# Performance work log

Measured on AMD Instinct MI355X. Metric: run time of the kernel, lower is better.

The kernel has to match this reference:

```python
import jax, jax.numpy as jnp
import numpy as np

N_NODES = 100000
N_EDGES = 3200000
IN_CH = 128
HID_CH = 128
OUT_CH = 64
N_GRAPHS = 128


def gcn_conv(x, edge_index, edge_weight, W, b):
    # x: [N, F_in]; edge_index: [2, E] (row=source j, col=target i); edge_weight: [E]
    N = x.shape[0]
    x = x @ W  # [N, F_out]
    # add self-loops with weight 1 (PyG GCNConv default, fill_value=1.0)
    loop = jnp.arange(N, dtype=edge_index.dtype)
    row = jnp.concatenate([edge_index[0], loop])
    col = jnp.concatenate([edge_index[1], loop])
    w = jnp.concatenate([edge_weight, jnp.ones((N,), dtype=x.dtype)])
    # symmetric normalization: deg computed at target (col)
    deg = jax.ops.segment_sum(w, col, num_segments=N)
    dinv = jnp.where(deg > 0, jax.lax.rsqrt(deg), 0.0)
    norm = dinv[row] * w * dinv[col]  # [E+N]
    msg = x[row] * norm[:, None]  # gather + scale
    out = jax.ops.segment_sum(msg, col, num_segments=N)  # scatter-add
    return out + b


def setup_inputs() -> dict:
    key = jax.random.key(0)
    ks = jax.random.split(key, 10)
    x = jax.random.normal(ks[0], (N_NODES, IN_CH), dtype=jnp.float32)
    edge_index = jax.random.randint(ks[1], (2, N_EDGES), 0, N_NODES, dtype=jnp.int64)
    edge_attr = jax.random.uniform(ks[2], (N_EDGES,), dtype=jnp.float32)
    batch = jnp.sort(jax.random.randint(ks[3], (N_NODES,), 0, N_GRAPHS, dtype=jnp.int64))
    # GCNConv weights (glorot) and zero bias, classifier xavier_normal + bias 0.1
    def glorot(k, fi, fo):
        s = jnp.sqrt(6.0 / (fi + fo))
        return jax.random.uniform(k, (fi, fo), minval=-s, maxval=s, dtype=jnp.float32)
    W1 = glorot(ks[4], IN_CH, HID_CH)
    b1 = jnp.zeros((HID_CH,), dtype=jnp.float32)
    W2 = glorot(ks[5], HID_CH, HID_CH)
    b2 = jnp.zeros((HID_CH,), dtype=jnp.float32)
    std = jnp.sqrt(2.0 / (HID_CH + OUT_CH))
    Wc = jax.random.normal(ks[6], (HID_CH, OUT_CH), dtype=jnp.float32) * std
    bc = jnp.full((OUT_CH,), 0.1, dtype=jnp.float32)
    return {"x": x, "edge_index": edge_index, "edge_attr": edge_attr,
            "batch": batch, "W1": W1, "b1": b1, "W2": W2, "b2": b2,
            "Wc": Wc, "bc": bc}


def reference(x, edge_index, edge_attr, batch, W1, b1, W2, b2, Wc, bc):
    h = jax.nn.relu(gcn_conv(x, edge_index, edge_attr, W1, b1))
    h = jax.nn.relu(gcn_conv(h, edge_index, edge_attr, W2, b2))
    pooled = jax.ops.segment_sum(h, batch, num_segments=N_GRAPHS)  # [G, HID]
    logits = pooled @ Wc + bc
    return jax.nn.sigmoid(logits)
```

## Files before the change

### kernel.cpp

```cpp
#include <hip/hip_runtime.h>
#include <hip/hip_bf16.h>
#include <hip/hip_fp16.h>


#define FEAT 128
#define OUTC 64
#define NB_SHIFT 8
#define BINSZ 256
#define CAP 9216
#define TILE_A 8192
#define CNT_STRIDE 16
#define LDW 136

typedef _Float16 half8 __attribute__((ext_vector_type(8)));
typedef float    f32x4 __attribute__((ext_vector_type(4)));
typedef int      iv4  __attribute__((ext_vector_type(4)));

__global__ __launch_bounds__(256) void bin_edges(const int* __restrict__ ei,
                                                 const float* __restrict__ ew,
                                                 int* __restrict__ binCnt,
                                                 int2* __restrict__ binned,
                                                 int E, int nbins) {
    extern __shared__ int2 sE[];
    __shared__ int kh[512], kb[512], kc[512], kg[512], ksc[512];
    int tid = threadIdx.x;
    int e0 = blockIdx.x * TILE_A;
    kh[tid] = 0; kh[tid + 256] = 0;
    kc[tid] = 0; kc[tid + 256] = 0;
    __syncthreads();
    for (int i = 0; i < TILE_A; i += 256) {
        int e = e0 + i + tid;
        if (e < E) atomicAdd(&kh[ei[E + e] >> NB_SHIFT], 1);
    }
    __syncthreads();
    int v0 = kh[tid], v1 = kh[tid + 256];
    ksc[tid] = v0; ksc[tid + 256] = v1;
    __syncthreads();
    for (int off = 1; off < 512; off <<= 1) {
        int a0 = (tid >= off) ? ksc[tid - off] : 0;
        int a1 = (tid + 256 >= off) ? ksc[tid + 256 - off] : 0;
        __syncthreads();
        ksc[tid] += a0; ksc[tid + 256] += a1;
        __syncthreads();
    }
    kb[tid] = ksc[tid] - v0;
    kb[tid + 256] = ksc[tid + 256] - v1;
    if (tid < nbins && v0 > 0) kg[tid] = atomicAdd(&binCnt[tid * CNT_STRIDE], v0);
    int t2 = tid + 256;
    if (t2 < nbins && v1 > 0) kg[t2] = atomicAdd(&binCnt[t2 * CNT_STRIDE], v1);
    __syncthreads();
    for (int i = 0; i < TILE_A; i += 256) {
        int e = e0 + i + tid;
        if (e < E) {
            int col = ei[E + e];
            int row = ei[e];
            unsigned short hs = __half_as_ushort(__float2half(ew[e]));
            int b = col >> NB_SHIFT;
            int p = kb[b] + atomicAdd(&kc[b], 1);
            int cl = col & (BINSZ - 1);
            sE[p] = make_int2((cl << 24) | row, (b << 16) | (int)hs);
        }
    }
    __syncthreads();
    int tot = ksc[511];
    for (int i = tid; i < tot; i += 256) {
        int2 m = sE[i];
        int b = ((unsigned)m.y) >> 16;
        int loc = kg[b] + (i - kb[b]);
        if (loc < CAP)
            binned[(size_t)b * CAP + loc] = make_int2(m.x, m.y & 0xFFFF);
    }
}

__global__ __launch_bounds__(256) void bin_sort_csr(int2* __restrict__ binned,
                                                    const int* __restrict__ binCnt,
                                                    int* __restrict__ offs,
                                                    int* __restrict__ cnt,
                                                    float* __restrict__ dinv, int N) {
    extern __shared__ int2 sE[];
    __shared__ float dsum[BINSZ];
    __shared__ int kh[BINSZ], kb[BINSZ], ksc[BINSZ];
    int tid = threadIdx.x, b = blockIdx.x;
    int node0 = b << NB_SHIFT;
    dsum[tid] = 0.f;
    kh[tid] = 0;
    __syncthreads();
    int ne = min(binCnt[b * CNT_STRIDE], CAP);
    int2* src = binned + (size_t)b * CAP;
    for (int i = tid; i < ne; i += 256) {
        int2 m = src[i];
        int cl = ((unsigned)m.x) >> 24;
        atomicAdd(&kh[cl], 1);
        unsafeAtomicAdd(&dsum[cl], __half2float(__ushort_as_half((unsigned short)(m.y & 0xFFFF))));
    }
    __syncthreads();
    int v = kh[tid];
    ksc[tid] = v;
    __syncthreads();
    for (int off = 1; off < BINSZ; off <<= 1) {
        int t = (tid >= off) ? ksc[tid - off] : 0;
        __syncthreads();
        ksc[tid] += t;
        __syncthreads();
    }
    kb[tid] = ksc[tid] - v;
    kh[tid] = 0;
    __syncthreads();
    for (int i = tid; i < ne; i += 256) {
        int2 m = src[i];
        int cl = ((unsigned)m.x) >> 24;
        int p = kb[cl] + atomicAdd(&kh[cl], 1);
        int hw = m.y & 0xFFFF;
        sE[p] = make_int2(m.x & 0xFFFFFF, hw | (hw << 16));
    }
    __syncthreads();
    for (int i = tid; i < ne; i += 256) src[i] = sE[i];
    int node = node0 + tid;
    if (node < N) {
        offs[node] = b * CAP + kb[tid];
        cnt[node]  = kh[tid];
        dinv[node] = rsqrtf(1.0f + dsum[tid]);
    }
}

__global__ void wt_prep(const float* __restrict__ W, _Float16* __restrict__ Wt) {
    int i = blockIdx.x * 256 + threadIdx.x;
    int n = i >> 7, k = i & 127;
    Wt[(size_t)n * LDW + k] = (_Float16)W[(size_t)k * FEAT + n];
}

template<typename TIn>
__global__ __launch_bounds__(256) void gemm_mfma(const TIn* __restrict__ X,
                                                 const _Float16* __restrict__ Wt,
                                                 const float* __restrict__ dinv,
                                                 __half* __restrict__ Y, int N) {
    __shared__ _Float16 sWt[FEAT * LDW];
    int tid  = threadIdx.x;
    int row0 = blockIdx.x * 128;
    {
        const int4* src = (const int4*)Wt;
        int4* dst = (int4*)sWt;
        for (int i = tid; i < (FEAT * LDW) / 8; i += 256) dst[i] = src[i];
    }
    __syncthreads();

    int wave = tid >> 6;
    int lane = tid & 63;
    int m    = lane & 15;
    int quad = lane >> 4;

    f32x4 acc[2][8];
    #pragma unroll
    for (int rt = 0; rt < 2; ++rt)
        #pragma unroll
        for (int ct = 0; ct < 8; ++ct)
            acc[rt][ct] = (f32x4){0.f, 0.f, 0.f, 0.f};

    int rowA[2];
    rowA[0] = min(row0 + wave * 32 + m, N - 1);
    rowA[1] = min(row0 + wave * 32 + 16 + m, N - 1);

    #pragma unroll
    for (int kt = 0; kt < 4; ++kt) {
        int k0 = kt * 32;
        half8 a[2];
        #pragma unroll
        for (int rt = 0; rt < 2; ++rt) {
            if constexpr (sizeof(TIn) == 4) {
                const float4* p = (const float4*)((const float*)X + (size_t)rowA[rt] * FEAT + k0 + quad * 8);
                float4 f0 = p[0], f1 = p[1];
                half8 h;
                h[0] = (_Float16)f0.x; h[1] = (_Float16)f0.y;
                h[2] = (_Float16)f0.z; h[3] = (_Float16)f0.w;
                h[4] = (_Float16)f1.x; h[5] = (_Float16)f1.y;
                h[6] = (_Float16)f1.z; h[7] = (_Float16)f1.w;
                a[rt] = h;
            } else {
                a[rt] = *(const half8*)((const _Float16*)X + (size_t)rowA[rt] * FEAT + k0 + quad * 8);
            }
        }
        #pragma unroll
        for (int ct = 0; ct < 8; ++ct) {
            half8 b = *(const half8*)&sWt[(ct * 16 + m) * LDW + k0 + quad * 8];
            acc[0][ct] = __builtin_amdgcn_mfma_f32_16x16x32_f16(a[0], b, acc[0][ct], 0, 0, 0);
            acc[1][ct] = __builtin_amdgcn_mfma_f32_16x16x32_f16(a[1], b, acc[1][ct], 0, 0, 0);
        }
    }

    #pragma unroll
    for (int rt = 0; rt < 2; ++rt) {
        int lr0 = wave * 32 + rt * 16 + quad * 4;
        #pragma unroll
        for (int r = 0; r < 4; ++r) {
            int gr = row0 + lr0 + r;
            if (gr < N) {
                float d = dinv[gr];
                #pragma unroll
                for (int ct = 0; ct < 8; ++ct)
                    Y[(size_t)gr * FEAT + ct * 16 + m] = __float2half(d * acc[rt][ct][r]);
            }
        }
    }
}

__global__ __launch_bounds__(256) void agg_kernel(const __half* __restrict__ Y,
                                                  const int2* __restrict__ elist,
                                                  const int* __restrict__ offs,
                                                  const int* __restrict__ cnt,
                                                  const float* __restrict__ dinv,
                                                  const float* __restrict__ bias,
                                                  __half* __restrict__ Out, int N) {
    int node = blockIdx.x * 4 + (threadIdx.x >> 6);
    int lane = threadIdx.x & 63;
    if (node >= N) return;
    int grp = lane >> 4;
    int fl  = lane & 15;
    int c = cnt[node];
    const int2* meta = elist + offs[node];

    __half2 z = __floats2half2_rn(0.f, 0.f);
    __half2 a0 = z, a1 = z, a2 = z, a3 = z;
    __half2 b0 = z, b1 = z, b2 = z, b3 = z;

    if (grp == 0) {
        int4 sv = ((const int4*)(Y + (size_t)node * FEAT))[fl];
        a0 = *(const __half2*)&sv.x; a1 = *(const __half2*)&sv.y;
        a2 = *(const __half2*)&sv.z; a3 = *(const __half2*)&sv.w;
    }

    for (int t = 0; t < c; t += 8) {
        int eA = t + grp;
        int eB = t + 4 + grp;
        int2 mA = (eA < c) ? meta[eA] : make_int2(node, 0);
        int2 mB = (eB < c) ? meta[eB] : make_int2(node, 0);
        int4 vA = *(const int4*)(Y + (size_t)mA.x * FEAT + fl * 8);
        int4 vB = *(const int4*)(Y + (size_t)mB.x * FEAT + fl * 8);
        __half2 wA = *(const __half2*)&mA.y;
        __half2 wB = *(const __half2*)&mB.y;
        a0 = __hfma2(wA, *(const __half2*)&vA.x, a0);
        a1 = __hfma2(wA, *(const __half2*)&vA.y, a1);
        a2 = __hfma2(wA, *(const __half2*)&vA.z, a2);
        a3 = __hfma2(wA, *(const __half2*)&vA.w, a3);
        b0 = __hfma2(wB, *(const __half2*)&vB.x, b0);
        b1 = __hfma2(wB, *(const __half2*)&vB.y, b1);
        b2 = __hfma2(wB, *(const __half2*)&vB.z, b2);
        b3 = __hfma2(wB, *(const __half2*)&vB.w, b3);
    }

    float2 F0 = __half22float2(a0), F1 = __half22float2(a1);
    float2 F2 = __half22float2(a2), F3 = __half22float2(a3);
    {
        float2 t0 = __half22float2(b0), t1 = __half22float2(b1);
        float2 t2 = __half22float2(b2), t3 = __half22float2(b3);
        F0.x += t0.x; F0.y += t0.y; F1.x += t1.x; F1.y += t1.y;
        F2.x += t2.x; F2.y += t2.y; F3.x += t3.x; F3.y += t3.y;
    }
    float f[8] = {F0.x, F0.y, F1.x, F1.y, F2.x, F2.y, F3.x, F3.y};
    #pragma unroll
    for (int i = 0; i < 8; ++i) {
        f[i] += __shfl_xor(f[i], 16);
        f[i] += __shfl_xor(f[i], 32);
    }
    if (grp == 0) {
        float d = dinv[node];
        int c0 = fl * 8;
        float4 bo0 = *(const float4*)(bias + c0);
        float4 bo1 = *(const float4*)(bias + c0 + 4);
        __half2 p01 = __floats2half2_rn(fmaxf(d * f[0] + bo0.x, 0.f), fmaxf(d * f[1] + bo0.y, 0.f));
        __half2 p23 = __floats2half2_rn(fmaxf(d * f[2] + bo0.z, 0.f), fmaxf(d * f[3] + bo0.w, 0.f));
        __half2 p45 = __floats2half2_rn(fmaxf(d * f[4] + bo1.x, 0.f), fmaxf(d * f[5] + bo1.y, 0.f));
        __half2 p67 = __floats2half2_rn(fmaxf(d * f[6] + bo1.z, 0.f), fmaxf(d * f[7] + bo1.w, 0.f));
        iv4 ov = { *(int*)&p01, *(int*)&p23, *(int*)&p45, *(int*)&p67 };
        *(iv4*)(Out + (size_t)node * FEAT + c0) = ov;
    }
}

__global__ void pool_kernel(const __half* __restrict__ H, const int* __restrict__ batch,
                            float* __restrict__ pooled, int N, int chunk) {
    int f  = threadIdx.x;
    int n0 = blockIdx.x * chunk;
    if (n0 >= N) return;
    int n1 = min(n0 + chunk, N);
    float acc = 0.f;
    int cur = batch[n0];
    for (int n = n0; n < n1; ++n) {
        int g = batch[n];
        if (g != cur) {
            unsafeAtomicAdd(&pooled[cur * FEAT + f], acc);
            acc = 0.f;
            cur = g;
        }
        acc += __half2float(H[(size_t)n * FEAT + f]);
    }
    unsafeAtomicAdd(&pooled[cur * FEAT + f], acc);
}

__global__ void classify_kernel(const float* __restrict__ pooled, const float* __restrict__ Wc,
                                const float* __restrict__ bc, float* __restrict__ out) {
    int g = blockIdx.x;
    int c = threadIdx.x;
    float acc = bc[c];
    const float* pr = pooled + g * FEAT;
    for (int k = 0; k < FEAT; ++k) acc += pr[k] * Wc[k * OUTC + c];
    out[g * OUTC + c] = 1.0f / (1.0f + expf(-acc));
}

extern "C" void kernel_launch(void* const* d_in, const int* in_sizes, int n_in,
                              void* d_out, int out_size, void* d_ws, size_t ws_size,
                              hipStream_t stream) {
    const float* x     = (const float*)d_in[0];
    const int*   ei    = (const int*)d_in[1];
    const float* ew    = (const float*)d_in[2];
    const int*   batch = (const int*)d_in[3];
    const float* W1    = (const float*)d_in[4];
    const float* b1    = (const float*)d_in[5];
    const float* W2    = (const float*)d_in[6];
    const float* b2    = (const float*)d_in[7];
    const float* Wc    = (const float*)d_in[8];
    const float* bc    = (const float*)d_in[9];
    float* out = (float*)d_out;

    const int N = in_sizes[0] / FEAT;
    const int E = in_sizes[2];
    const int G = out_size / OUTC;
    const int nbins = (N + BINSZ - 1) / BINSZ;

    char* w = (char*)d_ws;
    size_t off = 0;
    auto alloc = [&](size_t bytes) {
        void* p = w + off;
        off = (off + bytes + 255) & ~(size_t)255;
        return p;
    };
    float*     dinv   = (float*)alloc((size_t)N * 4);
    int*       cnt    = (int*)alloc((size_t)N * 4);
    int*       offs   = (int*)alloc((size_t)N * 4);
    int*       binCnt = (int*)alloc((size_t)nbins * CNT_STRIDE * 4);
    int2*      binned = (int2*)alloc((size_t)nbins * CAP * 8);
    __half*    bufY   = (__half*)alloc((size_t)N * FEAT * 2);
    __half*    bufH   = (__half*)alloc((size_t)N * FEAT * 2);
    float*     pooled = (float*)alloc((size_t)G * FEAT * 4);
    _Float16*  wt1    = (_Float16*)alloc((size_t)FEAT * LDW * 2);
    _Float16*  wt2    = (_Float16*)alloc((size_t)FEAT * LDW * 2);
    (void)ws_size;

    hipMemsetAsync(binCnt, 0, (size_t)nbins * CNT_STRIDE * 4, stream);
    hipMemsetAsync(pooled, 0, (size_t)G * FEAT * 4, stream);

    bin_edges<<<(E + TILE_A - 1) / TILE_A, 256, (size_t)TILE_A * sizeof(int2), stream>>>(ei, ew, binCnt, binned, E, nbins);
    bin_sort_csr<<<nbins, 256, (size_t)CAP * sizeof(int2), stream>>>(binned, binCnt, offs, cnt, dinv, N);
    wt_prep<<<64, 256, 0, stream>>>(W1, wt1);
    wt_prep<<<64, 256, 0, stream>>>(W2, wt2);

    const int gemm_blocks = (N + 127) / 128;
    const int agg_blocks  = (N + 3) / 4;

    gemm_mfma<float><<<gemm_blocks, 256, 0, stream>>>(x, wt1, dinv, bufY, N);
    agg_kernel<<<agg_blocks, 256, 0, stream>>>(bufY, binned, offs, cnt, dinv, b1, bufH, N);
    gemm_mfma<__half><<<gemm_blocks, 256, 0, stream>>>(bufH, wt2, dinv, bufY, N);
    agg_kernel<<<agg_blocks, 256, 0, stream>>>(bufY, binned, offs, cnt, dinv, b2, bufH, N);

    const int chunk = 128;
    pool_kernel<<<(N + chunk - 1) / chunk, FEAT, 0, stream>>>(bufH, batch, pooled, N, chunk);
    classify_kernel<<<G, OUTC, 0, stream>>>(pooled, Wc, bc, out);
}
```

Baseline: 510.7 us.

## Replace two-pass binned edge sort with atomic histogram, scan and scatter CSR build

```diff
diff --git a/kernel.cpp b/kernel.cpp
--- a/kernel.cpp
+++ b/kernel.cpp
@@ -5,127 +5,116 @@
 
 #define FEAT 128
 #define OUTC 64
-#define NB_SHIFT 8
-#define BINSZ 256
-#define CAP 9216
-#define TILE_A 8192
-#define CNT_STRIDE 16
-#define LDW 136
+#define CHUNK 2048
 
 typedef _Float16 half8 __attribute__((ext_vector_type(8)));
 typedef float    f32x4 __attribute__((ext_vector_type(4)));
 typedef int      iv4  __attribute__((ext_vector_type(4)));
 
-__global__ __launch_bounds__(256) void bin_edges(const int* __restrict__ ei,
-                                                 const float* __restrict__ ew,
-                                                 int* __restrict__ binCnt,
-                                                 int2* __restrict__ binned,
-                                                 int E, int nbins) {
-    extern __shared__ int2 sE[];
-    __shared__ int kh[512], kb[512], kc[512], kg[512], ksc[512];
+__global__ __launch_bounds__(256) void k_hist(const int* __restrict__ ei,
+                                              const float* __restrict__ ew,
+                                              int* __restrict__ deg,
+                                              float* __restrict__ wsum, int E) {
+    int stride = gridDim.x * 256;
+    for (int e = blockIdx.x * 256 + threadIdx.x; e < E; e += stride) {
+        int col = ei[E + e];
+        atomicAdd(&deg[col], 1);
+        unsafeAtomicAdd(&wsum[col], ew[e]);
+    }
+}
+
+__global__ __launch_bounds__(512) void k_chunksum(const int* __restrict__ deg,
+                                                  int* __restrict__ chunkSum, int N) {
+    __shared__ int ts[512];
     int tid = threadIdx.x;
-    int e0 = blockIdx.x * TILE_A;
-    kh[tid] = 0; kh[tid + 256] = 0;
-    kc[tid] = 0; kc[tid + 256] = 0;
+    int base = blockIdx.x * CHUNK + tid * 4;
+    int s = 0;
+    #pragma unroll
+    for (int j = 0; j < 4; ++j)
+        if (base + j < N) s += deg[base + j];
+    ts[tid] = s;
     __syncthreads();
-    for (int i = 0; i < TILE_A; i += 256) {
-        int e = e0 + i + tid;
-        if (e < E) atomicAdd(&kh[ei[E + e] >> NB_SHIFT], 1);
-    }
+    for (int off = 256; off > 0; off >>= 1) {
+        if (tid < off) ts[tid] += ts[tid + off];
+        __syncthreads();
+    }
+    if (tid == 0) chunkSum[blockIdx.x] = ts[0];
+}
+
+__global__ __launch_bounds__(64) void k_scanchunks(const int* __restrict__ chunkSum,
+                                                   int* __restrict__ chunkBase, int NC) {
+    __shared__ int ts[64];
+    int tid = threadIdx.x;
+    int v = (tid < NC) ? chunkSum[tid] : 0;
+    ts[tid] = v;
     __syncthreads();
-    int v0 = kh[tid], v1 = kh[tid + 256];
-    ksc[tid] = v0; ksc[tid + 256] = v1;
+    for (int off = 1; off < 64; off <<= 1) {
+        int a = (tid >= off) ? ts[tid - off] : 0;
+        __syncthreads();
+        ts[tid] += a;
+        __syncthreads();
+    }
+    if (tid < NC) chunkBase[tid] = ts[tid] - v;
+}
+
+__global__ __launch_bounds__(512) void k_offs(const int* __restrict__ deg,
+                                              const float* __restrict__ wsum,
+                                              const int* __restrict__ chunkBase,
+                                              int* __restrict__ offs,
+                                              int* __restrict__ cur,
+                                              float* __restrict__ dinv, int N) {
+    __shared__ int ts[512];
+    int tid = threadIdx.x;
+    int base = blockIdx.x * CHUNK + tid * 4;
+    int d[4] = {0, 0, 0, 0};
+    #pragma unroll
+    for (int j = 0; j < 4; ++j)
+        if (base + j < N) d[j] = deg[base + j];
+    int s = d[0] + d[1] + d[2] + d[3];
+    ts[tid] = s;
     __syncthreads();
     for (int off = 1; off < 512; off <<= 1) {
-        int a0 = (tid >= off) ? ksc[tid - off] : 0;
-        int a1 = (tid + 256 >= off) ? ksc[tid + 256 - off] : 0;
-        __syncthreads();
-        ksc[tid] += a0; ksc[tid + 256] += a1;
-        __syncthreads();
-    }
-    kb[tid] = ksc[tid] - v0;
-    kb[tid + 256] = ksc[tid + 256] - v1;
-    if (tid < nbins && v0 > 0) kg[tid] = atomicAdd(&binCnt[tid * CNT_STRIDE], v0);
-    int t2 = tid + 256;
-    if (t2 < nbins && v1 > 0) kg[t2] = atomicAdd(&binCnt[t2 * CNT_STRIDE], v1);
-    __syncthreads();
-    for (int i = 0; i < TILE_A; i += 256) {
-        int e = e0 + i + tid;
-        if (e < E) {
-            int col = ei[E + e];
-            int row = ei[e];
-            unsigned short hs = __half_as_ushort(__float2half(ew[e]));
-            int b = col >> NB_SHIFT;
-            int p = kb[b] + atomicAdd(&kc[b], 1);
-            int cl = col & (BINSZ - 1);
-            sE[p] = make_int2((cl << 24) | row, (b << 16) | (int)hs);
-        }
-    }
-    __syncthreads();
-    int tot = ksc[511];
-    for (int i = tid; i < tot; i += 256) {
-        int2 m = sE[i];
-        int b = ((unsigned)m.y) >> 16;
-        int loc = kg[b] + (i - kb[b]);
-        if (loc < CAP)
-            binned[(size_t)b * CAP + loc] = make_int2(m.x, m.y & 0xFFFF);
-    }
-}
-
-__global__ __launch_bounds__(256) void bin_sort_csr(int2* __restrict__ binned,
-                                                    const int* __restrict__ binCnt,
-                                                    int* __restrict__ offs,
-                                                    int* __restrict__ cnt,
-                                                    float* __restrict__ dinv, int N) {
-    extern __shared__ int2 sE[];
-    __shared__ float dsum[BINSZ];
-    __shared__ int kh[BINSZ], kb[BINSZ], ksc[BINSZ];
-    int tid = threadIdx.x, b = blockIdx.x;
-    int node0 = b << NB_SHIFT;
-    dsum[tid] = 0.f;
-    kh[tid] = 0;
-    __syncthreads();
-    int ne = min(binCnt[b * CNT_STRIDE], CAP);
-    int2* src = binned + (size_t)b * CAP;
-    for (int i = tid; i < ne; i += 256) {
-        int2 m = src[i];
-        int cl = ((unsigned)m.x) >> 24;
-        atomicAdd(&kh[cl], 1);
-        unsafeAtomicAdd(&dsum[cl], __half2float(__ushort_as_half((unsigned short)(m.y & 0xFFFF))));
-    }
-    __syncthreads();
-    int v = kh[tid];
-    ksc[tid] = v;
-    __syncthreads();
-    for (int off = 1; off < BINSZ; off <<= 1) {
-        int t = (tid >= off) ? ksc[tid - off] : 0;
-        __syncthreads();
-        ksc[tid] += t;
-        __syncthreads();
-    }
-    kb[tid] = ksc[tid] - v;
-    kh[tid] = 0;
-    __syncthreads();
-    for (int i = tid; i < ne; i += 256) {
-        int2 m = src[i];
-        int cl = ((unsigned)m.x) >> 24;
-        int p = kb[cl] + atomicAdd(&kh[cl], 1);
-        int hw = m.y & 0xFFFF;
-        sE[p] = make_int2(m.x & 0xFFFFFF, hw | (hw << 16));
-    }
-    __syncthreads();
-    for (int i = tid; i < ne; i += 256) src[i] = sE[i];
-    int node = node0 + tid;
-    if (node < N) {
-        offs[node] = b * CAP + kb[tid];
-        cnt[node]  = kh[tid];
-        dinv[node] = rsqrtf(1.0f + dsum[tid]);
-    }
-}
-
-__global__ void wt_prep(const float* __restrict__ W, _Float16* __restrict__ Wt) {
+        int a = (tid >= off) ? ts[tid - off] : 0;
+        __syncthreads();
+        ts[tid] += a;
+        __syncthreads();
+    }
+    int o = chunkBase[blockIdx.x] + ts[tid] - s;
+    #pragma unroll
+    for (int j = 0; j < 4; ++j) {
+        int n = base + j;
+        if (n < N) {
+            offs[n] = o;
+            cur[n]  = o;
+            dinv[n] = rsqrtf(1.0f + wsum[n]);
+            o += d[j];
+        }
+    }
+}
+
+__global__ __launch_bounds__(256) void k_scatter(const int* __restrict__ ei,
+                                                 const float* __restrict__ ew,
+                                                 int* __restrict__ cur,
+                                                 int2* __restrict__ elist, int E) {
+    int stride = gridDim.x * 256;
+    for (int e = blockIdx.x * 256 + threadIdx.x; e < E; e += stride) {
+        int col = ei[E + e];
+        int row = ei[e];
+        unsigned short hs = __half_as_ushort(__float2half(ew[e]));
+        int pos = atomicAdd(&cur[col], 1);
+        elist[pos] = make_int2(row, (int)hs | ((int)hs << 16));
+    }
+}
+
+#define LDW 136
+__global__ void wt_prep(const float* __restrict__ W1, const float* __restrict__ W2,
+                        _Float16* __restrict__ Wt1, _Float16* __restrict__ Wt2) {
     int i = blockIdx.x * 256 + threadIdx.x;
-    int n = i >> 7, k = i & 127;
+    int sel = i >> 14;
+    int r = i & 16383;
+    int n = r >> 7, k = r & 127;
+    const float* W = sel ? W2 : W1;
+    _Float16* Wt = sel ? Wt2 : Wt1;
     Wt[(size_t)n * LDW + k] = (_Float16)W[(size_t)k * FEAT + n];
 }
 
@@ -323,7 +312,7 @@
     const int N = in_sizes[0] / FEAT;
     const int E = in_sizes[2];
     const int G = out_size / OUTC;
-    const int nbins = (N + BINSZ - 1) / BINSZ;
+    const int NC = (N + CHUNK - 1) / CHUNK;
 
     char* w = (char*)d_ws;
     size_t off = 0;
@@ -332,33 +321,38 @@
         off = (off + bytes + 255) & ~(size_t)255;
         return p;
     };
-    float*     dinv   = (float*)alloc((size_t)N * 4);
-    int*       cnt    = (int*)alloc((size_t)N * 4);
-    int*       offs   = (int*)alloc((size_t)N * 4);
-    int*       binCnt = (int*)alloc((size_t)nbins * CNT_STRIDE * 4);
-    int2*      binned = (int2*)alloc((size_t)nbins * CAP * 8);
-    __half*    bufY   = (__half*)alloc((size_t)N * FEAT * 2);
-    __half*    bufH   = (__half*)alloc((size_t)N * FEAT * 2);
-    float*     pooled = (float*)alloc((size_t)G * FEAT * 4);
-    _Float16*  wt1    = (_Float16*)alloc((size_t)FEAT * LDW * 2);
-    _Float16*  wt2    = (_Float16*)alloc((size_t)FEAT * LDW * 2);
+    int*       deg     = (int*)alloc((size_t)N * 8);
+    float*     wsum    = (float*)(deg + N);
+    int*       offs    = (int*)alloc((size_t)N * 4);
+    int*       cur     = (int*)alloc((size_t)N * 4);
+    float*     dinv    = (float*)alloc((size_t)N * 4);
+    int*       chunkS  = (int*)alloc((size_t)NC * 4 * 2);
+    int*       chunkB  = chunkS + NC;
+    int2*      elist   = (int2*)alloc((size_t)E * 8);
+    __half*    bufY    = (__half*)alloc((size_t)N * FEAT * 2);
+    __half*    bufH    = (__half*)alloc((size_t)N * FEAT * 2);
+    float*     pooled  = (float*)alloc((size_t)G * FEAT * 4);
+    _Float16*  wt1     = (_Float16*)alloc((size_t)FEAT * LDW * 2);
+    _Float16*  wt2     = (_Float16*)alloc((size_t)FEAT * LDW * 2);
     (void)ws_size;
 
-    hipMemsetAsync(binCnt, 0, (size_t)nbins * CNT_STRIDE * 4, stream);
+    hipMemsetAsync(deg, 0, (size_t)N * 8, stream);
     hipMemsetAsync(pooled, 0, (size_t)G * FEAT * 4, stream);
 
-    bin_edges<<<(E + TILE_A - 1) / TILE_A, 256, (size_t)TILE_A * sizeof(int2), stream>>>(ei, ew, binCnt, binned, E, nbins);
-    bin_sort_csr<<<nbins, 256, (size_t)CAP * sizeof(int2), stream>>>(binned, binCnt, offs, cnt, dinv, N);
-    wt_prep<<<64, 256, 0, stream>>>(W1, wt1);
-    wt_prep<<<64, 256, 0, stream>>>(W2, wt2);
+    k_hist<<<2048, 256, 0, stream>>>(ei, ew, deg, wsum, E);
+    wt_prep<<<128, 256, 0, stream>>>(W1, W2, wt1, wt2);
+    k_chunksum<<<NC, 512, 0, stream>>>(deg, chunkS, N);
+    k_scanchunks<<<1, 64, 0, stream>>>(chunkS, chunkB, NC);
+    k_offs<<<NC, 512, 0, stream>>>(deg, wsum, chunkB, offs, cur, dinv, N);
+    k_scatter<<<2048, 256, 0, stream>>>(ei, ew, cur, elist, E);
 
     const int gemm_blocks = (N + 127) / 128;
     const int agg_blocks  = (N + 3) / 4;
 
     gemm_mfma<float><<<gemm_blocks, 256, 0, stream>>>(x, wt1, dinv, bufY, N);
-    agg_kernel<<<agg_blocks, 256, 0, stream>>>(bufY, binned, offs, cnt, dinv, b1, bufH, N);
+    agg_kernel<<<agg_blocks, 256, 0, stream>>>(bufY, elist, offs, deg, dinv, b1, bufH, N);
     gemm_mfma<__half><<<gemm_blocks, 256, 0, stream>>>(bufH, wt2, dinv, bufY, N);
-    agg_kernel<<<agg_blocks, 256, 0, stream>>>(bufY, binned, offs, cnt, dinv, b2, bufH, N);
+    agg_kernel<<<agg_blocks, 256, 0, stream>>>(bufY, elist, offs, deg, dinv, b2, bufH, N);
 
     const int chunk = 128;
     pool_kernel<<<(N + chunk - 1) / chunk, FEAT, 0, stream>>>(bufH, batch, pooled, N, chunk);
```

Result: slower. 973.8 us (+90.7%).
